# Optimization experiments

Hardware: AMD Instinct MI355X
Metric: run time of the kernel (lower is better)

Reference implementation:

```python
import jax, jax.numpy as jnp
import numpy as np

BLANK = 36
NEG = -1e30  # stand-in for -inf that stays NaN-free under logaddexp


def _ctc_loss(logits, targets, input_lengths, target_lengths):
    """CTC loss (reduction='mean', matching torch.nn.CTCLoss semantics:
    per-sample loss divided by target_length, then mean over batch).
    logits: [B, T, C] raw scores; targets: [B*L] flattened labels (fixed L per sample).
    """
    B, T, C = logits.shape
    L = targets.shape[0] // B
    tgt = targets.reshape(B, L)
    S = 2 * L + 1  # extended label length: blank-interleaved

    # log_softmax over classes, then time-major [T, B, C]
    lp = jnp.transpose(jax.nn.log_softmax(logits, axis=-1), (1, 0, 2))

    # extended targets: [blank, t1, blank, t2, ..., blank]  -> [B, S]
    ext = jnp.full((B, S), BLANK, dtype=tgt.dtype).at[:, 1::2].set(tgt)

    # gather log-probs of extended labels: [T, B, S]
    lp_ext = lp[:, jnp.arange(B)[:, None], ext]

    # positions beyond 2*target_len are invalid
    valid = jnp.arange(S)[None, :] < (2 * target_lengths[:, None] + 1)  # [B, S]
    # skip transition s-2 -> s allowed only if ext[s] != blank and ext[s] != ext[s-2]
    skip_ok = (ext != BLANK) & jnp.concatenate(
        [jnp.zeros((B, 2), bool), ext[:, 2:] != ext[:, :-2]], axis=1)

    end_idx = 2 * target_lengths  # index of final blank; [B]

    def final_ll(alpha):
        e1 = jnp.take_along_axis(alpha, end_idx[:, None], axis=1)[:, 0]
        e2 = jnp.take_along_axis(alpha, (end_idx - 1)[:, None], axis=1)[:, 0]
        return jnp.logaddexp(e1, e2)

    # t = 0 initialization
    alpha0 = jnp.full((B, S), NEG, logits.dtype)
    alpha0 = alpha0.at[:, 0].set(lp_ext[0, :, 0]).at[:, 1].set(lp_ext[0, :, 1])
    alpha0 = jnp.where(valid, alpha0, NEG)
    final0 = jnp.where(input_lengths == 1, final_ll(alpha0), NEG)

    pad1 = jnp.full((B, 1), NEG, logits.dtype)
    pad2 = jnp.full((B, 2), NEG, logits.dtype)

    def step(carry, inp):
        alpha, final = carry
        t, lpe = inp  # lpe: [B, S]
        a1 = jnp.concatenate([pad1, alpha[:, :-1]], axis=1)
        a2 = jnp.where(skip_ok, jnp.concatenate([pad2, alpha[:, :-2]], axis=1), NEG)
        new = jnp.logaddexp(jnp.logaddexp(alpha, a1), a2) + lpe
        new = jnp.where(valid, new, NEG)
        final = jnp.where(input_lengths == t + 1, final_ll(new), final)
        return (new, final), None

    (_, final), _ = jax.lax.scan(step, (alpha0, final0),
                                 (jnp.arange(1, T), lp_ext[1:]))
    return jnp.mean(-final / target_lengths.astype(logits.dtype))


def setup_inputs() -> dict:
    key = jax.random.key(0)
    k1, k2 = jax.random.split(key)
    B, T, C, L = 2048, 256, 37, 16
    logits = jax.random.normal(k1, (B, T, C), dtype=jnp.float32)
    targets = jax.random.randint(k2, (B * L,), 0, 36, dtype=jnp.int32)  # never blank
    input_lengths = jnp.full((B,), T, dtype=jnp.int32)
    target_lengths = jnp.full((B,), L, dtype=jnp.int32)
    return {"logits": logits, "targets": targets,
            "input_lengths": input_lengths, "target_lengths": target_lengths}


def reference(logits, targets, input_lengths, target_lengths):
    return _ctc_loss(logits, targets, input_lengths, target_lengths)
```

## Files before the change

kernel.cpp:

```cpp
#include <hip/hip_runtime.h>

#define BLANK 36
#define NEG -1e30f
#define CC 37
#define LOG37 3.6109179126442243f

__device__ __forceinline__ float logaddexp_f(float a, float b) {
    float m = fmaxf(a, b);
    float d = fabsf(a - b);
    return m + __logf(1.0f + __expf(-d));
}

#define DPP0(src, ctrl) __builtin_amdgcn_update_dpp(0, (src), (ctrl), 0xf, 0xf, true)
#define DPPM(old, src, ctrl) __builtin_amdgcn_update_dpp((old), (src), (ctrl), 0xf, 0xf, false)

__global__ __launch_bounds__(128, 4) void ctc_fused_ab_kernel(
    const float* __restrict__ logits,
    const int*   __restrict__ targets,
    const int*   __restrict__ input_lengths,
    const int*   __restrict__ target_lengths,
    float*       __restrict__ per_sample,
    int B, int T, int L)
{
    __shared__ float lds[2 * 2368 + 66];
    const int lane = threadIdx.x & 63;
    const int wib  = threadIdx.x >> 6;
    const int b    = blockIdx.x;

    float* Xw   = lds + wib * 2368;
    float* exch = lds + 4736;

    const int S = 2 * L + 1;
    const int tlen_s = __builtin_amdgcn_readfirstlane(target_lengths[b]);
    const int ilen_s = __builtin_amdgcn_readfirstlane(input_lengths[b]);
    const int end_s  = 2 * tlen_s;
    const int halfT  = T >> 1;
    const int NC     = T >> 6;
    const int NCh    = NC >> 1;

    const int st = (wib == 0) ? lane : (63 - lane);
    int ext_w = BLANK;
    if (st < S && (st & 1)) ext_w = targets[b * L + (st >> 1)];
    const int exo = __shfl_up(ext_w, 2);
    float kf;
    if (wib == 0)
        kf = ((st >= 2) && (st < S) && (ext_w != BLANK) && (ext_w != exo)) ? 1.0f : 0.0f;
    else
        kf = ((st + 2 < S) && (exo != BLANK) && (exo != ext_w)) ? 1.0f : 0.0f;

    const bool c16 = ((lane & 31) == 16);
    const bool c17 = ((lane & 31) == 17);
    const bool c32 = (lane == 32);
    const bool c33 = (lane == 33);

    const float4* src = (const float4*)(logits + (size_t)b * T * CC);

    auto SHIFTS = [&](float x, float& a1, float& a2) {
        const int xi  = __float_as_int(x);
        const int s1  = DPP0(xi, 0x111);
        const int s2  = DPP0(xi, 0x112);
        const int b15 = DPP0(xi, 0x142);
        const int b31 = DPP0(xi, 0x143);
        const int y15 = DPP0(s1, 0x142);
        const int y31 = DPP0(s1, 0x143);
        a1 = __int_as_float(c16 ? b15 : (c32 ? b31 : s1));
        a2 = __int_as_float(c16 ? y15 : (c17 ? b15 : (c32 ? y31 : (c33 ? b31 : s2))));
    };

    auto RESCALE = [&](float& x, float& racc) {
        float m = x;
        m = fmaxf(m, __int_as_float(DPPM(__float_as_int(m), __float_as_int(m), 0x111)));
        m = fmaxf(m, __int_as_float(DPPM(__float_as_int(m), __float_as_int(m), 0x112)));
        m = fmaxf(m, __int_as_float(DPPM(__float_as_int(m), __float_as_int(m), 0x114)));
        m = fmaxf(m, __int_as_float(DPPM(__float_as_int(m), __float_as_int(m), 0x118)));
        m = fmaxf(m, __int_as_float(DPPM(__float_as_int(m), __float_as_int(m), 0x142)));
        m = fmaxf(m, __int_as_float(DPPM(__float_as_int(m), __float_as_int(m), 0x143)));
        float gm = __int_as_float(__builtin_amdgcn_readlane(__float_as_int(m), 63));
        gm = fmaxf(gm, 1e-30f);
        x *= (1.0f / gm);
        racc += __logf(gm);
    };

    auto SOFTMAX = [&](float* Xn) {
        float xr[CC];
        const float* row = Xn + lane * CC;
        #pragma unroll
        for (int c2 = 0; c2 < CC; ++c2) xr[c2] = row[c2];
        float m = xr[0];
        #pragma unroll
        for (int c2 = 1; c2 < CC; ++c2) m = fmaxf(m, xr[c2]);
        float ss = 0.0f;
        #pragma unroll
        for (int c2 = 0; c2 < CC; ++c2) { xr[c2] = __expf(xr[c2] - m); ss += xr[c2]; }
        const float inv = 37.0f / ss;
        float* wrow = Xn + lane * CC;
        #pragma unroll
        for (int c2 = 0; c2 < CC; ++c2) wrow[c2] = xr[c2] * inv;
    };

    auto STAGE = [&](const float4* s2g) {
        float4* dst = (float4*)Xw;
        #pragma unroll
        for (int k = 0; k < 9; ++k) dst[k * 64 + lane] = s2g[k * 64 + lane];
        if (lane < 16) dst[576 + lane] = s2g[576 + lane];
        __builtin_amdgcn_s_waitcnt(0);
    };

    float z = 0.0f, racc = 0.0f, capv = NEG;
    float pw[16];

    if (wib == 0) {
        STAGE(src);
        SOFTMAX(Xw);
        __builtin_amdgcn_s_waitcnt(0);
        #pragma unroll 1
        for (int c = 0; c < NCh; ++c) {
            const bool more = (c + 1 < NCh);
            float4 f0 = {}, f1 = {}, f2 = {}, f3 = {}, f4 = {},
                   f5 = {}, f6 = {}, f7 = {}, f8 = {}, f9 = {};
            if (more) {
                const float4* s2g = src + (size_t)(c + 1) * 592;
                f0 = s2g[lane];       f1 = s2g[64 + lane];  f2 = s2g[128 + lane];
                f3 = s2g[192 + lane]; f4 = s2g[256 + lane]; f5 = s2g[320 + lane];
                f6 = s2g[384 + lane]; f7 = s2g[448 + lane]; f8 = s2g[512 + lane];
                if (lane < 16) f9 = s2g[576 + lane];
            }
            const int tbase = c << 6;
            #pragma unroll
            for (int j = 0; j < 16; ++j) pw[j] = Xw[j * CC + ext_w];
            #pragma unroll
            for (int r = 0; r < 64; ++r) {
                const float p = pw[r & 15];
                if (r + 16 < 64) pw[r & 15] = Xw[(r + 16) * CC + ext_w];
                if (c == 0 && r == 0) {
                    z = (lane <= 1) ? p : 0.0f;
                    if (ilen_s == 1) capv = __logf(fmaxf(z, 1e-35f)) - LOG37;
                } else {
                    float a1, a2;
                    SHIFTS(z, a1, a2);
                    z = fmaf(kf, a2, z + a1) * p;
                    const int tt = tbase + r;
                    if (ilen_s == tt + 1)
                        capv = __logf(fmaxf(z, 1e-35f)) + racc - (float)(tt + 1) * LOG37;
                }
                if ((r & 15) == 15) RESCALE(z, racc);
            }
            if (more) {
                float4* dst = (float4*)Xw;
                dst[lane] = f0;       dst[64 + lane] = f1;  dst[128 + lane] = f2;
                dst[192 + lane] = f3; dst[256 + lane] = f4; dst[320 + lane] = f5;
                dst[384 + lane] = f6; dst[448 + lane] = f7; dst[512 + lane] = f8;
                if (lane < 16) dst[576 + lane] = f9;
                __builtin_amdgcn_s_waitcnt(0);
                SOFTMAX(Xw);
                __builtin_amdgcn_s_waitcnt(0);
            }
        }
    } else {
        STAGE(src + (size_t)(NC - 1) * 592);
        SOFTMAX(Xw);
        __builtin_amdgcn_s_waitcnt(0);
        const int il1 = ilen_s - 1;
        #pragma unroll 1
        for (int i = 0; i < NCh; ++i) {
            const bool more = (i + 1 < NCh);
            float4 f0 = {}, f1 = {}, f2 = {}, f3 = {}, f4 = {},
                   f5 = {}, f6 = {}, f7 = {}, f8 = {}, f9 = {};
            if (more) {
                const float4* s2g = src + (size_t)(NC - 2 - i) * 592;
                f0 = s2g[lane];       f1 = s2g[64 + lane];  f2 = s2g[128 + lane];
                f3 = s2g[192 + lane]; f4 = s2g[256 + lane]; f5 = s2g[320 + lane];
                f6 = s2g[384 + lane]; f7 = s2g[448 + lane]; f8 = s2g[512 + lane];
                if (lane < 16) f9 = s2g[576 + lane];
            }
            const int cbase = (NC - 1 - i) << 6;
            #pragma unroll
            for (int j = 0; j < 16; ++j) pw[j] = Xw[(63 - j) * CC + ext_w];
            #pragma unroll
            for (int r = 0; r < 64; ++r) {
                const int tt = cbase + 63 - r;
                if (tt == il1) {
                    z = (lane == 63 - end_s || lane == 64 - end_s) ? 1.0f : 0.0f;
                    racc = 0.0f;
                }
                const float p = pw[r & 15];
                if (r + 16 < 64) pw[r & 15] = Xw[(63 - (r + 16)) * CC + ext_w];
                const float u = z * p;
                float a1, a2;
                SHIFTS(u, a1, a2);
                z = fmaf(kf, a2, u + a1);
                if ((r & 15) == 15) RESCALE(z, racc);
            }
            if (more) {
                float4* dst = (float4*)Xw;
                dst[lane] = f0;       dst[64 + lane] = f1;  dst[128 + lane] = f2;
                dst[192 + lane] = f3; dst[256 + lane] = f4; dst[320 + lane] = f5;
                dst[384 + lane] = f6; dst[448 + lane] = f7; dst[512 + lane] = f8;
                if (lane < 16) dst[576 + lane] = f9;
                __builtin_amdgcn_s_waitcnt(0);
                SOFTMAX(Xw);
                __builtin_amdgcn_s_waitcnt(0);
            }
        }
    }

    __syncthreads();
    if (wib == 1) {
        exch[63 - lane] = z;
        if (lane == 0) exch[64] = racc;
    }
    __syncthreads();
    if (wib == 0) {
        const float bs = exch[lane];
        const float rb = exch[64];
        float prod = z * bs;
        #pragma unroll
        for (int o = 32; o > 0; o >>= 1) prod += __shfl_xor(prod, o);
        float final_v;
        if (ilen_s <= halfT) {
            const float e1 = __shfl(capv, end_s);
            const float e2 = __shfl(capv, end_s - 1);
            final_v = logaddexp_f(e1, e2);
        } else {
            final_v = __logf(fmaxf(prod, 1e-37f)) + racc + rb - (float)ilen_s * LOG37;
        }
        if (lane == 0) per_sample[b] = -final_v / (float)tlen_s;
    }
}

__global__ __launch_bounds__(256) void lse_kernel(
    const float* __restrict__ logits, float* __restrict__ denom, int N)
{
    __shared__ float lds[256 * CC];
    const int lane = threadIdx.x & 63;
    const int wib  = threadIdx.x >> 6;
    const int wave = blockIdx.x * 4 + wib;
    const long long row0 = (long long)wave * 64;
    if (row0 >= N) return;
    const int wbase = wib * 64 * CC;
    const float4* src4 = (const float4*)(logits + row0 * CC);
    const long long n4_remaining = ((long long)N * CC - row0 * CC) / 4;
    float4* lds4 = (float4*)(lds + wbase);
    #pragma unroll
    for (int k = 0; k < 10; ++k) {
        const int idx = k * 64 + lane;
        if (idx < 592 && idx < n4_remaining) lds4[idx] = src4[idx];
    }
    __builtin_amdgcn_s_waitcnt(0);
    const long long row = row0 + lane;
    if (row >= N) return;
    const float* x = lds + wbase + lane * CC;
    float m = x[0];
    #pragma unroll
    for (int c = 1; c < CC; ++c) m = fmaxf(m, x[c]);
    float s = 0.0f;
    #pragma unroll
    for (int c = 0; c < CC; ++c) s += __expf(x[c] - m);
    denom[row] = m + __logf(s);
}

__global__ __launch_bounds__(256) void ctc_alpha2_kernel(
    const float* __restrict__ logits, const float* __restrict__ denom,
    const int* __restrict__ targets, const int* __restrict__ input_lengths,
    const int* __restrict__ target_lengths, float* __restrict__ per_sample,
    int B, int T, int L)
{
    const int wave = (int)((blockIdx.x * blockDim.x + threadIdx.x) >> 6);
    const int lane = threadIdx.x & 63;
    if (wave >= B) return;
    const int b = wave;
    const int S = 2 * L + 1;
    const int tlen = target_lengths[b];
    const int ilen = input_lengths[b];
    const int end_idx = 2 * tlen;
    int ext_s = BLANK;
    if (lane < S && (lane & 1)) ext_s = targets[b * L + (lane >> 1)];
    const int ext_sm2 = __shfl_up(ext_s, 2);
    const bool skip_ok = (lane < S) && (lane >= 2) && (ext_s != BLANK) && (ext_s != ext_sm2);
    const bool valid = lane < (2 * tlen + 1);
    const float* lg = logits + (size_t)b * T * CC;
    const float* dn = denom + (size_t)b * T;
    float x_cur = lg[ext_s];
    float d_cur = dn[0];
    float x_nx = (T > 1) ? lg[CC + ext_s] : 0.0f;
    float d_nx = (T > 1) ? dn[1] : 0.0f;
    float final_v = NEG;
    float alpha = (valid && lane <= 1) ? (x_cur - d_cur) : NEG;
    if (ilen == 1) {
        const float e1 = __shfl(alpha, end_idx);
        const float e2 = __shfl(alpha, end_idx - 1);
        final_v = logaddexp_f(e1, e2);
    }
    for (int tt = 1; tt < T; ++tt) {
        x_cur = x_nx; d_cur = d_nx;
        if (tt + 1 < T) {
            x_nx = lg[(size_t)(tt + 1) * CC + ext_s];
            d_nx = dn[tt + 1];
        }
        const float lpe = x_cur - d_cur;
        float a1 = __shfl_up(alpha, 1);
        if (lane == 0) a1 = NEG;
        float a2 = __shfl_up(alpha, 2);
        if (!skip_ok) a2 = NEG;
        const float m = fmaxf(fmaxf(alpha, a1), a2);
        const float s = __expf(alpha - m) + __expf(a1 - m) + __expf(a2 - m);
        const float na = m + __logf(s) + lpe;
        alpha = valid ? na : NEG;
        if (ilen == tt + 1) {
            const float e1 = __shfl(alpha, end_idx);
            const float e2 = __shfl(alpha, end_idx - 1);
            final_v = logaddexp_f(e1, e2);
        }
    }
    if (lane == 0) per_sample[b] = -final_v / (float)tlen;
}

__global__ __launch_bounds__(256) void ctc_alpha_mono_kernel(
    const float* __restrict__ logits, const int* __restrict__ targets,
    const int* __restrict__ input_lengths, const int* __restrict__ target_lengths,
    float* __restrict__ per_sample, int B, int T, int L)
{
    const int wave = (int)((blockIdx.x * blockDim.x + threadIdx.x) >> 6);
    const int lane = threadIdx.x & 63;
    if (wave >= B) return;
    const int b = wave;
    const int S = 2 * L + 1;
    const int tlen = target_lengths[b];
    const int ilen = input_lengths[b];
    const int end_idx = 2 * tlen;
    int ext_s = BLANK;
    if (lane < S && (lane & 1)) ext_s = targets[b * L + (lane >> 1)];
    const int ext_sm2 = __shfl_up(ext_s, 2);
    const bool skip_ok = (lane < S) && (lane >= 2) && (ext_s != BLANK) && (ext_s != ext_sm2);
    const bool valid = lane < (2 * tlen + 1);
    const float* lg = logits + (size_t)b * T * CC;
    float alpha = NEG, final_v = NEG;
    for (int t = 0; t < T; ++t) {
        float x = (lane < CC) ? lg[t * CC + lane] : -3.0e38f;
        float mx = x;
        #pragma unroll
        for (int o = 32; o > 0; o >>= 1) mx = fmaxf(mx, __shfl_xor(mx, o));
        float e = (lane < CC) ? __expf(x - mx) : 0.0f;
        float se = e;
        #pragma unroll
        for (int o = 32; o > 0; o >>= 1) se += __shfl_xor(se, o);
        const float lp = x - mx - __logf(se);
        const float lpe = __shfl(lp, ext_s);
        float newa;
        if (t == 0) {
            newa = (lane <= 1) ? lpe : NEG;
        } else {
            float a1 = __shfl_up(alpha, 1);
            if (lane == 0) a1 = NEG;
            float a2 = __shfl_up(alpha, 2);
            if (!skip_ok) a2 = NEG;
            newa = logaddexp_f(logaddexp_f(alpha, a1), a2) + lpe;
        }
        if (!valid) newa = NEG;
        alpha = newa;
        if (ilen == t + 1) {
            const float e1 = __shfl(alpha, end_idx);
            const float e2 = __shfl(alpha, end_idx - 1);
            final_v = logaddexp_f(e1, e2);
        }
    }
    if (lane == 0) per_sample[b] = -final_v / (float)tlen;
}

__global__ __launch_bounds__(256) void reduce_mean_kernel(
    const float* __restrict__ ps, float* __restrict__ out, int B)
{
    float s = 0.0f;
    for (int i = threadIdx.x; i < B; i += 256) s += ps[i];
    #pragma unroll
    for (int o = 32; o > 0; o >>= 1) s += __shfl_xor(s, o);
    __shared__ float sm[4];
    const int w = threadIdx.x >> 6, l = threadIdx.x & 63;
    if (l == 0) sm[w] = s;
    __syncthreads();
    if (threadIdx.x == 0) {
        out[0] = (sm[0] + sm[1] + sm[2] + sm[3]) / (float)B;
    }
}

extern "C" void kernel_launch(void* const* d_in, const int* in_sizes, int n_in,
                              void* d_out, int out_size, void* d_ws, size_t ws_size,
                              hipStream_t stream) {
    const float* logits         = (const float*)d_in[0];
    const int*   targets        = (const int*)d_in[1];
    const int*   input_lengths  = (const int*)d_in[2];
    const int*   target_lengths = (const int*)d_in[3];

    const int B = in_sizes[2];
    const int L = in_sizes[1] / B;
    const int T = in_sizes[0] / (B * CC);
    const long long N = (long long)B * T;

    float* per_sample = (float*)d_ws;
    float* scratch    = per_sample + B;
    float* out        = (float*)d_out;

    const size_t ws_mid = ((size_t)B + (size_t)N) * sizeof(float);
    const int nblocks_alpha = (B * 64 + 255) / 256;
    const long long nwaves = (N + 63) / 64;

    if ((T % 128 == 0) && T >= 128 && L <= 31 && ws_size >= (size_t)B * sizeof(float)) {
        ctc_fused_ab_kernel<<<B, 128, 0, stream>>>(
            logits, targets, input_lengths, target_lengths, per_sample, B, T, L);
    } else if (ws_size >= ws_mid && T >= 2) {
        lse_kernel<<<(int)((nwaves + 3) / 4), 256, 0, stream>>>(logits, scratch, (int)N);
        ctc_alpha2_kernel<<<nblocks_alpha, 256, 0, stream>>>(
            logits, scratch, targets, input_lengths, target_lengths, per_sample, B, T, L);
    } else {
        ctc_alpha_mono_kernel<<<nblocks_alpha, 256, 0, stream>>>(
            logits, targets, input_lengths, target_lengths, per_sample, B, T, L);
    }
    reduce_mean_kernel<<<1, 256, 0, stream>>>(per_sample, out, B);
}
```

Measured before the change: 136.4 us.

## Pack two samples per wavefront in fused forward-backward CTC kernel

Adds a new kernel that maps two batch samples onto each 64-lane wavefront, one per 32-lane half. Wave 0 runs the forward alpha pass and wave 1 the backward beta pass, meeting at the midpoint. Since S=33 fits into 32 lanes plus one scalar extra state, this halves the block count and removes the idle lanes of the one-sample-per-wave layout. In exchange it needs intricate half-wave DPP shifts and restricts the path to L<=16 and even B.

```diff
diff --git a/kernel.cpp b/kernel.cpp
--- a/kernel.cpp
+++ b/kernel.cpp
@@ -13,6 +13,240 @@
 
 #define DPP0(src, ctrl) __builtin_amdgcn_update_dpp(0, (src), (ctrl), 0xf, 0xf, true)
 #define DPPM(old, src, ctrl) __builtin_amdgcn_update_dpp((old), (src), (ctrl), 0xf, 0xf, false)
+
+__global__ __launch_bounds__(128, 2) void ctc_fused_ab2_kernel(
+    const float* __restrict__ logits,
+    const int*   __restrict__ targets,
+    const int*   __restrict__ input_lengths,
+    const int*   __restrict__ target_lengths,
+    float*       __restrict__ per_sample,
+    int B, int T, int L)
+{
+    __shared__ float lds[2 * 2368 + 72];
+    const int lane = threadIdx.x & 63;
+    const int wib  = threadIdx.x >> 6;
+    const int h    = lane >> 5;
+    const int l    = lane & 31;
+    const int b0   = blockIdx.x * 2;
+    const int bme  = b0 + h;
+
+    float* Xw   = lds + wib * 2368;
+    float* Xh   = Xw + h * 1184;
+    float* exch = lds + 4736;
+
+    const int halfT = T >> 1;
+    const int NCh   = halfT >> 5;
+
+    const int tl_lane  = target_lengths[bme];
+    const int il_lane  = input_lengths[bme];
+    const int end_lane = 2 * tl_lane;
+    const int s_ilA = __builtin_amdgcn_readlane(il_lane, 0);
+    const int s_ilB = __builtin_amdgcn_readlane(il_lane, 32);
+
+    int ext_w = BLANK;
+    if (!(l & 1)) {
+        int ti = (wib == 0) ? (l >> 1) : (15 - (l >> 1));
+        if (ti >= L) ti = L - 1;
+        if (ti < 0) ti = 0;
+        ext_w = targets[bme * L + ti];
+    }
+    const int exo = __shfl_up(ext_w, 2);
+    float kf;
+    if (wib == 0)
+        kf = (l >= 2 && ext_w != BLANK && ext_w != exo) ? 1.0f : 0.0f;
+    else
+        kf = ((33 - l) <= 2 * L && exo != BLANK && exo != ext_w) ? 1.0f : 0.0f;
+
+    const bool c16 = (l == 16);
+    const bool c17 = (l == 17);
+    const bool cz0 = (l == 0);
+    const int bcast_addr = (((lane & 32) | 31) << 2);
+
+    const float4* baseH4 = (const float4*)(logits + (size_t)bme * T * CC);
+    const float* pwp = Xh + ext_w;
+    const float* pbp = Xh + 36;
+
+    auto SHIFTS = [&](float x, float inj, float& a1, float& a2) {
+        const int xi  = __float_as_int(x);
+        const int s1  = DPP0(xi, 0x111);
+        const int s2  = DPP0(xi, 0x112);
+        const int b15 = DPP0(xi, 0x142);
+        const int y15 = DPP0(s1, 0x142);
+        a1 = cz0 ? inj : __int_as_float(c16 ? b15 : s1);
+        a2 = __int_as_float(c16 ? y15 : (c17 ? b15 : s2));
+    };
+
+    auto RESCALE = [&](float& x, float& x2, float& racc) {
+        float m = fmaxf(x, x2);
+        m = fmaxf(m, __int_as_float(DPPM(__float_as_int(m), __float_as_int(m), 0x111)));
+        m = fmaxf(m, __int_as_float(DPPM(__float_as_int(m), __float_as_int(m), 0x112)));
+        m = fmaxf(m, __int_as_float(DPPM(__float_as_int(m), __float_as_int(m), 0x114)));
+        m = fmaxf(m, __int_as_float(DPPM(__float_as_int(m), __float_as_int(m), 0x118)));
+        m = fmaxf(m, __int_as_float(DPPM(__float_as_int(m), __float_as_int(m), 0x142)));
+        float gm = __int_as_float(__builtin_amdgcn_ds_bpermute(bcast_addr, __float_as_int(m)));
+        gm = fmaxf(gm, 1e-30f);
+        const float inv = __builtin_amdgcn_rcpf(gm);
+        x *= inv; x2 *= inv;
+        racc += __logf(gm);
+    };
+
+    auto SOFTMAX = [&](float* Xn) {
+        float xr[CC];
+        const float* row = Xn + lane * CC;
+        #pragma unroll
+        for (int c2 = 0; c2 < CC; ++c2) xr[c2] = row[c2];
+        float m = xr[0];
+        #pragma unroll
+        for (int c2 = 1; c2 < CC; ++c2) m = fmaxf(m, xr[c2]);
+        float ss = 0.0f;
+        #pragma unroll
+        for (int c2 = 0; c2 < CC; ++c2) { xr[c2] = __expf(xr[c2] - m); ss += xr[c2]; }
+        const float inv = 37.0f / ss;
+        float* wrow = Xn + lane * CC;
+        #pragma unroll
+        for (int c2 = 0; c2 < CC; ++c2) wrow[c2] = xr[c2] * inv;
+    };
+
+    auto STAGE = [&](int tbase) {
+        const float4* s4 = baseH4 + ((tbase * CC) >> 2);
+        float4* d4 = (float4*)Xh;
+        #pragma unroll
+        for (int k = 0; k < 9; ++k) d4[k * 32 + l] = s4[k * 32 + l];
+        if (l < 8) d4[288 + l] = s4[288 + l];
+        __builtin_amdgcn_s_waitcnt(0);
+    };
+
+    float z = 0.0f, zx = 0.0f, racc = 0.0f, capv = NEG;
+    float pw[16], pb[16];
+
+    if (wib == 0) {
+        STAGE(0);
+        SOFTMAX(Xw);
+        __builtin_amdgcn_s_waitcnt(0);
+        #pragma unroll 1
+        for (int c = 0; c < NCh; ++c) {
+            const bool more = (c + 1 < NCh);
+            float4 f0 = {}, f1 = {}, f2 = {}, f3 = {}, f4 = {},
+                   f5 = {}, f6 = {}, f7 = {}, f8 = {}, f9 = {};
+            if (more) {
+                const float4* s4 = baseH4 + ((((c + 1) << 5) * CC) >> 2);
+                f0 = s4[l];       f1 = s4[32 + l];  f2 = s4[64 + l];
+                f3 = s4[96 + l];  f4 = s4[128 + l]; f5 = s4[160 + l];
+                f6 = s4[192 + l]; f7 = s4[224 + l]; f8 = s4[256 + l];
+                if (l < 8) f9 = s4[288 + l];
+            }
+            #pragma unroll
+            for (int j = 0; j < 16; ++j) { pw[j] = pwp[j * CC]; pb[j] = pbp[j * CC]; }
+            #pragma unroll
+            for (int r = 0; r < 32; ++r) {
+                const float p   = pw[r & 15];
+                const float pbv = pb[r & 15];
+                if (r < 16) { pw[r & 15] = pwp[(r + 16) * CC]; pb[r & 15] = pbp[(r + 16) * CC]; }
+                if (c == 0 && r == 0) {
+                    z  = cz0 ? p : 0.0f;
+                    zx = pbv;
+                } else {
+                    float a1, a2;
+                    SHIFTS(z, zx, a1, a2);
+                    z = fmaf(kf, a2, z + a1) * p;
+                    zx *= pbv;
+                }
+                const int tt = (c << 5) + r;
+                if (s_ilA == tt + 1 || s_ilB == tt + 1) {
+                    const float cv = __logf(fmaxf(z, 1e-35f)) + racc - (float)(tt + 1) * LOG37;
+                    capv = (il_lane == tt + 1) ? cv : capv;
+                }
+                if ((r & 15) == 15) RESCALE(z, zx, racc);
+            }
+            if (more) {
+                float4* d4 = (float4*)Xh;
+                d4[l] = f0;       d4[32 + l] = f1;  d4[64 + l] = f2;
+                d4[96 + l] = f3;  d4[128 + l] = f4; d4[160 + l] = f5;
+                d4[192 + l] = f6; d4[224 + l] = f7; d4[256 + l] = f8;
+                if (l < 8) d4[288 + l] = f9;
+                __builtin_amdgcn_s_waitcnt(0);
+                SOFTMAX(Xw);
+                __builtin_amdgcn_s_waitcnt(0);
+            }
+        }
+    } else {
+        STAGE(T - 32);
+        SOFTMAX(Xw);
+        __builtin_amdgcn_s_waitcnt(0);
+        #pragma unroll 1
+        for (int i = 0; i < NCh; ++i) {
+            const bool more = (i + 1 < NCh);
+            float4 f0 = {}, f1 = {}, f2 = {}, f3 = {}, f4 = {},
+                   f5 = {}, f6 = {}, f7 = {}, f8 = {}, f9 = {};
+            if (more) {
+                const float4* s4 = baseH4 + (((T - (i + 2) * 32) * CC) >> 2);
+                f0 = s4[l];       f1 = s4[32 + l];  f2 = s4[64 + l];
+                f3 = s4[96 + l];  f4 = s4[128 + l]; f5 = s4[160 + l];
+                f6 = s4[192 + l]; f7 = s4[224 + l]; f8 = s4[256 + l];
+                if (l < 8) f9 = s4[288 + l];
+            }
+            const int tbase = T - (i + 1) * 32;
+            #pragma unroll
+            for (int j = 0; j < 16; ++j) { pw[j] = pwp[(31 - j) * CC]; pb[j] = pbp[(31 - j) * CC]; }
+            #pragma unroll
+            for (int r = 0; r < 32; ++r) {
+                const int tt = tbase + 31 - r;
+                if (s_ilA == tt + 1 || s_ilB == tt + 1) {
+                    const bool cond = (il_lane == tt + 1);
+                    const float zi = (l == 31 - end_lane || l == 32 - end_lane) ? 1.0f : 0.0f;
+                    z    = cond ? zi : z;
+                    zx   = cond ? ((end_lane == 32) ? 1.0f : 0.0f) : zx;
+                    racc = cond ? 0.0f : racc;
+                }
+                const float p   = pw[r & 15];
+                const float pbv = pb[r & 15];
+                if (r < 16) { pw[r & 15] = pwp[(15 - r) * CC]; pb[r & 15] = pbp[(15 - r) * CC]; }
+                const float u  = z * p;
+                const float uE = zx * pbv;
+                float a1, a2;
+                SHIFTS(u, uE, a1, a2);
+                z  = fmaf(kf, a2, u + a1);
+                zx = uE;
+                if ((r & 15) == 15) RESCALE(z, zx, racc);
+            }
+            if (more) {
+                float4* d4 = (float4*)Xh;
+                d4[l] = f0;       d4[32 + l] = f1;  d4[64 + l] = f2;
+                d4[96 + l] = f3;  d4[128 + l] = f4; d4[160 + l] = f5;
+                d4[192 + l] = f6; d4[224 + l] = f7; d4[256 + l] = f8;
+                if (l < 8) d4[288 + l] = f9;
+                __builtin_amdgcn_s_waitcnt(0);
+                SOFTMAX(Xw);
+                __builtin_amdgcn_s_waitcnt(0);
+            }
+        }
+    }
+
+    __syncthreads();
+    if (wib == 1) {
+        exch[h * 35 + (31 - l)] = z;
+        if (l == 0) { exch[h * 35 + 32] = zx; exch[h * 35 + 33] = racc; }
+    }
+    __syncthreads();
+    if (wib == 0) {
+        const float bs = exch[h * 35 + l + 1];
+        float prod = z * bs + (cz0 ? zx * exch[h * 35] : 0.0f);
+        #pragma unroll
+        for (int o = 16; o > 0; o >>= 1) prod += __shfl_xor(prod, o);
+        const float rb = exch[h * 35 + 33];
+        int i1 = (lane & 32) + end_lane - 1;
+        if (i1 < 0) i1 = 0;
+        int i2 = i1 - 1;
+        if (i2 < 0) i2 = 0;
+        const float e1 = __shfl(capv, i1);
+        const float e2 = __shfl(capv, i2);
+        const float fcap = logaddexp_f(e1, e2);
+        const float fmid = __logf(fmaxf(prod, 1e-37f)) + racc + rb
+                           - (float)il_lane * LOG37;
+        const float final_v = (il_lane <= halfT) ? fcap : fmid;
+        if (l == 0) per_sample[bme] = -final_v / (float)tl_lane;
+    }
+}
 
 __global__ __launch_bounds__(128, 4) void ctc_fused_ab_kernel(
     const float* __restrict__ logits,
@@ -404,7 +638,14 @@
     const int nblocks_alpha = (B * 64 + 255) / 256;
     const long long nwaves = (N + 63) / 64;
 
-    if ((T % 128 == 0) && T >= 128 && L <= 31 && ws_size >= (size_t)B * sizeof(float)) {
+    const bool ws_ok = ws_size >= (size_t)B * sizeof(float);
+    const bool fast2 = (B % 2 == 0) && (T % 64 == 0) && T >= 64 && L <= 16 && ws_ok;
+    const bool fast1 = (T % 128 == 0) && T >= 128 && L <= 31 && ws_ok;
+
+    if (fast2) {
+        ctc_fused_ab2_kernel<<<B / 2, 128, 0, stream>>>(
+            logits, targets, input_lengths, target_lengths, per_sample, B, T, L);
+    } else if (fast1) {
         ctc_fused_ab_kernel<<<B, 128, 0, stream>>>(
             logits, targets, input_lengths, target_lengths, per_sample, B, T, L);
     } else if (ws_size >= ws_mid && T >= 2) {
```

Measured after the change: 119.6 us. 1.14x faster.
